# Performance work log

Hardware: AMD Instinct MI355X
Metric: run time of the kernel (lower is better)

Reference implementation:

```python
import math
import jax, jax.numpy as jnp
import numpy as np

NQ, NK = 16384, 4096
QDIM, KDIM, MID = 512, 256, 256


def setup_inputs() -> dict:
    key = jax.random.key(0)
    k1, k2, k3, k4, k5, k6, k7, k8 = jax.random.split(key, 8)
    return {
        "global_embeddings": jax.random.normal(k1, (NQ, QDIM), dtype=jnp.float32),
        "substruct_embeddings": jax.random.normal(k2, (NK, KDIM), dtype=jnp.float32),
        "substruct_weight": jax.random.uniform(k3, (NK,), dtype=jnp.float32),
        "mask": jax.random.randint(k4, (NQ, NK), 0, 2, dtype=jnp.int32),
        "Wq": jax.random.normal(k5, (MID, QDIM), dtype=jnp.float32) / math.sqrt(QDIM),
        "bq": jax.random.normal(k6, (MID,), dtype=jnp.float32) * 0.01,
        "Wk": jax.random.normal(k7, (MID, KDIM), dtype=jnp.float32) / math.sqrt(KDIM),
        "bk": jax.random.normal(k8, (MID,), dtype=jnp.float32) * 0.01,
    }


def reference(global_embeddings, substruct_embeddings, substruct_weight, mask, Wq, bq, Wk, bk):
    # Q/K projections (torch Linear: x @ W.T + b)
    Q = global_embeddings @ Wq.T + bq            # [NQ, MID]
    K = substruct_embeddings @ Wk.T + bk         # [NK, MID]
    scores = (Q @ K.T) / math.sqrt(MID)          # [NQ, NK]
    scores = jnp.where(mask == 0, -jnp.inf, scores)
    attn = jax.nn.softmax(scores, axis=-1)       # row-wise stable softmax
    # torch.diag(w) @ E  ==  elementwise row scaling
    V = substruct_weight[:, None] * substruct_embeddings  # [NK, KDIM]
    return attn @ V                              # [NQ, KDIM]
```

## Files before the change

kernel.cpp:

```cpp
#include <hip/hip_runtime.h>
#include <hip/hip_bf16.h>

typedef __bf16 bf16_t;
typedef bf16_t bf16x8 __attribute__((ext_vector_type(8)));
typedef float  f32x4  __attribute__((ext_vector_type(4)));
typedef unsigned long long u64;
typedef unsigned int u32;

#define MFMA16(A,B,C) __builtin_amdgcn_mfma_f32_16x16x32_bf16((A),(B),(C),0,0,0)


static __device__ __forceinline__ void gl_lds16(const bf16_t* g, void* l) {
    __builtin_amdgcn_global_load_lds(
        (const __attribute__((address_space(1))) u32*)(const void*)g,
        (__attribute__((address_space(3))) u32*)l, 16, 0, 0);
}

template<int KA, bool SWZ>
__global__ __launch_bounds__(256)
void proj_kernel(const float* __restrict__ A, const float* __restrict__ W,
                 const float* __restrict__ b, bf16_t* __restrict__ C,
                 float scale)
{
    __shared__ bf16_t Alds[64][40];
    __shared__ bf16_t Wlds[256][40];

    const int t  = threadIdx.x;
    const int w  = t >> 6, l = t & 63, lr = l & 15, lg = l >> 4;
    const int m0 = blockIdx.x * 64;

    f32x4 acc[16];
#pragma unroll
    for (int tt = 0; tt < 16; ++tt) acc[tt] = (f32x4){0.f, 0.f, 0.f, 0.f};

    const int ar  = t >> 2;
    const int ac8 = (t & 3) * 8;

    for (int kb = 0; kb < KA / 32; ++kb) {
        {
            const float* ap = A + (size_t)(m0 + ar) * KA + kb * 32 + ac8;
            float4 a0 = *(const float4*)ap;
            float4 a1 = *(const float4*)(ap + 4);
            bf16x8 av;
            av[0]=(bf16_t)a0.x; av[1]=(bf16_t)a0.y; av[2]=(bf16_t)a0.z; av[3]=(bf16_t)a0.w;
            av[4]=(bf16_t)a1.x; av[5]=(bf16_t)a1.y; av[6]=(bf16_t)a1.z; av[7]=(bf16_t)a1.w;
            *(bf16x8*)&Alds[ar][ac8] = av;
        }
#pragma unroll
        for (int c = 0; c < 4; ++c) {
            int e8 = c * 256 + t;
            int wr = e8 >> 2, wc8 = (e8 & 3) * 8;
            const float* wp = W + (size_t)wr * KA + kb * 32 + wc8;
            float4 w0 = *(const float4*)wp;
            float4 w1 = *(const float4*)(wp + 4);
            bf16x8 wv;
            wv[0]=(bf16_t)w0.x; wv[1]=(bf16_t)w0.y; wv[2]=(bf16_t)w0.z; wv[3]=(bf16_t)w0.w;
            wv[4]=(bf16_t)w1.x; wv[5]=(bf16_t)w1.y; wv[6]=(bf16_t)w1.z; wv[7]=(bf16_t)w1.w;
            *(bf16x8*)&Wlds[wr][wc8] = wv;
        }
        __syncthreads();

        bf16x8 af = *(bf16x8*)&Alds[w * 16 + lr][lg * 8];
#pragma unroll
        for (int tt = 0; tt < 16; ++tt) {
            bf16x8 bfrag = *(bf16x8*)&Wlds[tt * 16 + lr][lg * 8];
            acc[tt] = MFMA16(af, bfrag, acc[tt]);
        }
        __syncthreads();
    }

#pragma unroll
    for (int tt = 0; tt < 16; ++tt) {
        int col = tt * 16 + lr;
        float bias = b[col];
#pragma unroll
        for (int r = 0; r < 4; ++r) {
            int row = m0 + w * 16 + lg * 4 + r;
            int colS = col;
            if (SWZ) colS = (((col >> 3) ^ (row & 7)) << 3) | (col & 7);
            C[(size_t)row * 256 + colS] = (bf16_t)((acc[tt][r] + bias) * scale);
        }
    }
}

__global__ __launch_bounds__(256)
void buildvt_kernel(const float* __restrict__ S, const float* __restrict__ wgt,
                    bf16_t* __restrict__ VT)
{
    int i = blockIdx.x * 256 + threadIdx.x;
    int d = i >> 12, k = i & 4095;
    int kt = (k & ~63) | (((((k >> 3) & 7) ^ (d & 7)) << 3)) | (k & 7);
    VT[i] = (bf16_t)(wgt[kt] * S[(size_t)kt * 256 + d]);
}

template<bool SPLIT>
__global__ __launch_bounds__(512, 2)
void attn_kernel(const bf16_t* __restrict__ Qb, const bf16_t* __restrict__ Kb,
                 const bf16_t* __restrict__ VT, const int* __restrict__ mask,
                 float* __restrict__ out, float* __restrict__ pacc,
                 float* __restrict__ pm, float* __restrict__ pl)
{
    __shared__ __align__(16) char Kraw[2][32768];
    __shared__ __align__(16) char Vraw[2][32768];

    const int t  = threadIdx.x;
    const int w  = t >> 6, l = t & 63, lr = l & 15, lg = l >> 4;
    const int qw = blockIdx.x * 128 + w * 16;
    const int half = SPLIT ? (int)blockIdx.y : 0;
    const int NT   = SPLIT ? 32 : 64;
    const int kb0  = half * NT;

    bf16x8 qf[8];
    {
        const bf16_t* qrow = Qb + (size_t)(qw + lr) * 256;
#pragma unroll
        for (int kk = 0; kk < 8; ++kk)
            qf[kk] = *(const bf16x8*)(qrow + kk * 32 + lg * 8);
    }

    bf16x8 vone;
#pragma unroll
    for (int j = 0; j < 8; ++j) vone[j] = (bf16_t)1.0f;

    f32x4 acc[16];
#pragma unroll
    for (int dt = 0; dt < 16; ++dt) acc[dt] = (f32x4){0.f, 0.f, 0.f, 0.f};
    f32x4 lacc = (f32x4){0.f, 0.f, 0.f, 0.f};
    float mrow = -1e30f;
    bf16x8 pa[2];

    char* const K0 = &Kraw[0][0];
    char* const K1 = &Kraw[1][0];
    char* const V0 = &Vraw[0][0];
    char* const V1 = &Vraw[1][0];

    auto stageK = [&](int kb, char* kd) {
#pragma unroll
        for (int i = 0; i < 4; ++i) {
            int row = w * 8 + i * 2 + (l >> 5);
            gl_lds16(Kb + (size_t)(kb * 64 + row) * 256 + (l & 31) * 8,
                     kd + (w * 8 + i * 2) * 512);
        }
    };
    auto stageV = [&](int kb, char* vd) {
#pragma unroll
        for (int i = 0; i < 4; ++i) {
            int d = w * 32 + i * 8 + (l >> 3);
            gl_lds16(VT + (size_t)d * 4096 + kb * 64 + (l & 7) * 8,
                     vd + (w * 32 + i * 8) * 128);
        }
    };

    auto qk = [&](char* kcur, f32x4 (&s)[4]) {
#pragma unroll
        for (int tt = 0; tt < 4; ++tt) {
            f32x4 sv = (f32x4){0.f, 0.f, 0.f, 0.f};
#pragma unroll
            for (int kk = 0; kk < 8; ++kk) {
                bf16x8 kf = *(bf16x8*)(kcur + (((tt * 16 + lr) * 512)
                                | ((((kk * 4 + lg) ^ (lr & 7)) << 4))));
                sv = MFMA16(kf, qf[kk], sv);
            }
            s[tt] = sv;
        }
    };

    auto pv = [&](char* vcur) {
        lacc = MFMA16(pa[0], vone, lacc);
        lacc = MFMA16(pa[1], vone, lacc);
#pragma unroll
        for (int dt = 0; dt < 16; ++dt) {
            int vrow = dt * 16 + lr;
            bf16x8 v0 = *(bf16x8*)(vcur + ((vrow * 128)
                            | ((((0 * 4 + lg) ^ (lr & 7)) << 4))));
            bf16x8 v1 = *(bf16x8*)(vcur + ((vrow * 128)
                            | ((((1 * 4 + lg) ^ (lr & 7)) << 4))));
            acc[dt] = MFMA16(pa[0], v0, acc[dt]);
            acc[dt] = MFMA16(pa[1], v1, acc[dt]);
        }
    };

    auto softmax = [&](int4 (&mv)[4], f32x4 (&s)[4]) {
#pragma unroll
        for (int tt = 0; tt < 4; ++tt) {
            s[tt][0] = mv[tt].x ? s[tt][0] : -1e30f;
            s[tt][1] = mv[tt].y ? s[tt][1] : -1e30f;
            s[tt][2] = mv[tt].z ? s[tt][2] : -1e30f;
            s[tt][3] = mv[tt].w ? s[tt][3] : -1e30f;
        }
        float bm;
        {
            f32x4 m4 = s[0];
#pragma unroll
            for (int tt = 1; tt < 4; ++tt) {
                m4[0] = fmaxf(m4[0], s[tt][0]);
                m4[1] = fmaxf(m4[1], s[tt][1]);
                m4[2] = fmaxf(m4[2], s[tt][2]);
                m4[3] = fmaxf(m4[3], s[tt][3]);
            }
            bm = fmaxf(fmaxf(m4[0], m4[1]), fmaxf(m4[2], m4[3]));
            bm = fmaxf(bm, __shfl_xor(bm, 16));
            bm = fmaxf(bm, __shfl_xor(bm, 32));
        }
        bool need = bm > mrow + 8.f;
        if (__any(need)) {
            float mn = fmaxf(mrow, bm);
            float fr = __expf(mrow - mn);
            mrow = mn;
            float frC[4];
#pragma unroll
            for (int r = 0; r < 4; ++r) frC[r] = __shfl(fr, lg * 4 + r);
#pragma unroll
            for (int r = 0; r < 4; ++r) {
                lacc[r] *= frC[r];
#pragma unroll
                for (int dt = 0; dt < 16; ++dt) acc[dt][r] *= frC[r];
            }
        }
#pragma unroll
        for (int tt = 0; tt < 4; ++tt)
#pragma unroll
            for (int r = 0; r < 4; ++r)
                s[tt][r] = __expf(s[tt][r] - mrow);

#pragma unroll
        for (int g = 0; g < 2; ++g) {
            u32 x0, x1, y0, y1;
            asm("v_cvt_pk_bf16_f32 %0, %1, %2"
                : "=v"(x0) : "v"(s[2 * g][0]), "v"(s[2 * g][1]));
            asm("v_cvt_pk_bf16_f32 %0, %1, %2"
                : "=v"(x1) : "v"(s[2 * g][2]), "v"(s[2 * g][3]));
            asm("v_cvt_pk_bf16_f32 %0, %1, %2"
                : "=v"(y0) : "v"(s[2 * g + 1][0]), "v"(s[2 * g + 1][1]));
            asm("v_cvt_pk_bf16_f32 %0, %1, %2"
                : "=v"(y1) : "v"(s[2 * g + 1][2]), "v"(s[2 * g + 1][3]));
            asm volatile("v_permlane32_swap_b32 %0, %1" : "+v"(x0), "+v"(y0));
            asm volatile("v_permlane32_swap_b32 %0, %1" : "+v"(x1), "+v"(y1));
            u32 sx0 = (u32)__shfl_xor((int)x0, 16);
            u32 sx1 = (u32)__shfl_xor((int)x1, 16);
            u32 sy0 = (u32)__shfl_xor((int)y0, 16);
            u32 sy1 = (u32)__shfl_xor((int)y1, 16);
            bool evn = (lg & 1) == 0;
            union { u32 uw[4]; bf16x8 v; } pu;
            pu.uw[0] = evn ? x0  : sy0;
            pu.uw[1] = evn ? x1  : sy1;
            pu.uw[2] = evn ? sx0 : y0;
            pu.uw[3] = evn ? sx1 : y1;
            pa[g] = pu.v;
        }
    };

    stageK(kb0, K0);
    stageV(kb0, V0);
    __syncthreads();
    {
        int4 mv[4];
#pragma unroll
        for (int tt = 0; tt < 4; ++tt)
            mv[tt] = *(const int4*)(mask + (size_t)(qw + lr) * 4096
                                    + kb0 * 64 + tt * 16 + lg * 4);
        f32x4 s[4];
        qk(K0, s);
        softmax(mv, s);
    }
    stageK(kb0 + 1, K1);
    __syncthreads();

    for (int tb = 0; tb < NT - 1; ++tb) {
        char* kQ = (tb & 1) ? K0 : K1;
        char* vP = (tb & 1) ? V1 : V0;
        char* kS = (tb & 1) ? K1 : K0;
        char* vS = (tb & 1) ? V0 : V1;
        const int kb = kb0 + tb;

        int4 mv[4];
#pragma unroll
        for (int tt = 0; tt < 4; ++tt)
            mv[tt] = *(const int4*)(mask + (size_t)(qw + lr) * 4096
                                    + (kb + 1) * 64 + tt * 16 + lg * 4);

        if (tb + 2 < NT) stageK(kb + 2, kS);
        stageV(kb + 1, vS);

        __builtin_amdgcn_s_setprio(1);
        f32x4 s[4];
        qk(kQ, s);
        pv(vP);
        __builtin_amdgcn_s_setprio(0);

        softmax(mv, s);

        __syncthreads();
    }

    {
        char* vP = ((NT - 1) & 1) ? V1 : V0;
        pv(vP);
    }

    if (SPLIT) {
        float* pa_ = pacc + (size_t)half * 16384 * 256;
#pragma unroll
        for (int r = 0; r < 4; ++r) {
            int row = qw + lg * 4 + r;
#pragma unroll
            for (int dt = 0; dt < 16; ++dt)
                pa_[(size_t)row * 256 + dt * 16 + lr] = acc[dt][r];
            if (lr == 0) pl[half * 16384 + row] = lacc[r];
        }
        if (l < 16) pm[half * 16384 + qw + lr] = mrow;
    } else {
#pragma unroll
        for (int r = 0; r < 4; ++r) {
            float inv = 1.0f / lacc[r];
#pragma unroll
            for (int dt = 0; dt < 16; ++dt)
                out[(size_t)(qw + lg * 4 + r) * 256 + dt * 16 + lr]
                    = acc[dt][r] * inv;
        }
    }
}

__global__ __launch_bounds__(256)
void combine_kernel(const float* __restrict__ pacc, const float* __restrict__ pm,
                    const float* __restrict__ pl, float* __restrict__ out)
{
    int idx = blockIdx.x * 256 + threadIdx.x;
    int row = idx >> 6, c4 = (idx & 63) * 4;
    float m0 = pm[row], m1 = pm[16384 + row];
    float l0 = pl[row], l1 = pl[16384 + row];
    float m  = fmaxf(m0, m1);
    float a  = __expf(m0 - m), b = __expf(m1 - m);
    float inv = 1.0f / (l0 * a + l1 * b);
    float4 x0 = *(const float4*)(pacc + (size_t)row * 256 + c4);
    float4 x1 = *(const float4*)(pacc + (size_t)16384 * 256 + (size_t)row * 256 + c4);
    float4 o;
    o.x = (x0.x * a + x1.x * b) * inv;
    o.y = (x0.y * a + x1.y * b) * inv;
    o.z = (x0.z * a + x1.z * b) * inv;
    o.w = (x0.w * a + x1.w * b) * inv;
    *(float4*)(out + (size_t)row * 256 + c4) = o;
}

extern "C" void kernel_launch(void* const* d_in, const int* in_sizes, int n_in,
                              void* d_out, int out_size, void* d_ws, size_t ws_size,
                              hipStream_t stream)
{
    const float* gE   = (const float*)d_in[0];
    const float* sE   = (const float*)d_in[1];
    const float* wgt  = (const float*)d_in[2];
    const int*   mask = (const int*)  d_in[3];
    const float* Wq   = (const float*)d_in[4];
    const float* bq   = (const float*)d_in[5];
    const float* Wk   = (const float*)d_in[6];
    const float* bk   = (const float*)d_in[7];
    float* out = (float*)d_out;

    char* ws = (char*)d_ws;
    bf16_t* Qb = (bf16_t*)ws;
    bf16_t* Kb = (bf16_t*)(ws + 8388608);
    bf16_t* VT = (bf16_t*)(ws + 10485760);
    float*  pacc = (float*)(ws + 12582912);
    float*  pm   = (float*)(ws + 46137344);
    float*  pl   = (float*)(ws + 46268416);
    const size_t need_full = 46399488;
    const size_t need_min  = 12582912;

    if (ws_size < need_min) return;

    proj_kernel<512, false><<<dim3(256, 1), 256, 0, stream>>>(gE, Wq, bq, Qb, 0.0625f);
    proj_kernel<256, true ><<<dim3(64, 1), 256, 0, stream>>>(sE, Wk, bk, Kb, 1.0f);
    buildvt_kernel<<<4096, 256, 0, stream>>>(sE, wgt, VT);

    if (ws_size >= need_full) {
        attn_kernel<true><<<dim3(128, 2), 512, 0, stream>>>(
            Qb, Kb, VT, mask, out, pacc, pm, pl);
        combine_kernel<<<4096, 256, 0, stream>>>(pacc, pm, pl, out);
    } else {
        attn_kernel<false><<<dim3(128, 1), 512, 0, stream>>>(
            Qb, Kb, VT, mask, out, nullptr, nullptr, nullptr);
    }
}
```

Baseline: 187.7 us.

## Shrink attention tiles to 64 queries and 32 keys with pre-tiled V layout

```diff
diff --git a/kernel.cpp b/kernel.cpp
--- a/kernel.cpp
+++ b/kernel.cpp
@@ -85,29 +85,32 @@
 
 __global__ __launch_bounds__(256)
 void buildvt_kernel(const float* __restrict__ S, const float* __restrict__ wgt,
-                    bf16_t* __restrict__ VT)
+                    bf16_t* __restrict__ VTg)
 {
     int i = blockIdx.x * 256 + threadIdx.x;
-    int d = i >> 12, k = i & 4095;
-    int kt = (k & ~63) | (((((k >> 3) & 7) ^ (d & 7)) << 3)) | (k & 7);
-    VT[i] = (bf16_t)(wgt[kt] * S[(size_t)kt * 256 + d]);
+    int kb = i >> 13;
+    int c  = (i >> 11) & 3;
+    int d  = (i >> 3) & 255;
+    int j  = i & 7;
+    int k  = kb * 32 + c * 8 + j;
+    VTg[i] = (bf16_t)(wgt[k] * S[(size_t)k * 256 + d]);
 }
 
 template<bool SPLIT>
-__global__ __launch_bounds__(512, 2)
+__global__ __launch_bounds__(256, 2)
 void attn_kernel(const bf16_t* __restrict__ Qb, const bf16_t* __restrict__ Kb,
-                 const bf16_t* __restrict__ VT, const int* __restrict__ mask,
+                 const bf16_t* __restrict__ VTg, const int* __restrict__ mask,
                  float* __restrict__ out, float* __restrict__ pacc,
                  float* __restrict__ pm, float* __restrict__ pl)
 {
-    __shared__ __align__(16) char Kraw[2][32768];
-    __shared__ __align__(16) char Vraw[2][32768];
+    __shared__ __align__(16) char Kraw[2][16384];
+    __shared__ __align__(16) char Vraw[2][16384];
 
     const int t  = threadIdx.x;
     const int w  = t >> 6, l = t & 63, lr = l & 15, lg = l >> 4;
-    const int qw = blockIdx.x * 128 + w * 16;
+    const int qw = blockIdx.x * 64 + w * 16;
     const int half = SPLIT ? (int)blockIdx.y : 0;
-    const int NT   = SPLIT ? 32 : 64;
+    const int NT   = SPLIT ? 64 : 128;
     const int kb0  = half * NT;
 
     bf16x8 qf[8];
@@ -127,7 +130,7 @@
     for (int dt = 0; dt < 16; ++dt) acc[dt] = (f32x4){0.f, 0.f, 0.f, 0.f};
     f32x4 lacc = (f32x4){0.f, 0.f, 0.f, 0.f};
     float mrow = -1e30f;
-    bf16x8 pa[2];
+    bf16x8 pa;
 
     char* const K0 = &Kraw[0][0];
     char* const K1 = &Kraw[1][0];
@@ -138,22 +141,21 @@
 #pragma unroll
         for (int i = 0; i < 4; ++i) {
             int row = w * 8 + i * 2 + (l >> 5);
-            gl_lds16(Kb + (size_t)(kb * 64 + row) * 256 + (l & 31) * 8,
+            gl_lds16(Kb + (size_t)(kb * 32 + row) * 256 + (l & 31) * 8,
                      kd + (w * 8 + i * 2) * 512);
         }
     };
     auto stageV = [&](int kb, char* vd) {
 #pragma unroll
         for (int i = 0; i < 4; ++i) {
-            int d = w * 32 + i * 8 + (l >> 3);
-            gl_lds16(VT + (size_t)d * 4096 + kb * 64 + (l & 7) * 8,
-                     vd + (w * 32 + i * 8) * 128);
-        }
-    };
-
-    auto qk = [&](char* kcur, f32x4 (&s)[4]) {
-#pragma unroll
-        for (int tt = 0; tt < 4; ++tt) {
+            gl_lds16(VTg + (size_t)kb * 8192 + w * 2048 + i * 512 + l * 8,
+                     vd + w * 4096 + i * 1024);
+        }
+    };
+
+    auto qk = [&](char* kcur, f32x4 (&s)[2]) {
+#pragma unroll
+        for (int tt = 0; tt < 2; ++tt) {
             f32x4 sv = (f32x4){0.f, 0.f, 0.f, 0.f};
 #pragma unroll
             for (int kk = 0; kk < 8; ++kk) {
@@ -166,23 +168,17 @@
     };
 
     auto pv = [&](char* vcur) {
-        lacc = MFMA16(pa[0], vone, lacc);
-        lacc = MFMA16(pa[1], vone, lacc);
+        lacc = MFMA16(pa, vone, lacc);
 #pragma unroll
         for (int dt = 0; dt < 16; ++dt) {
-            int vrow = dt * 16 + lr;
-            bf16x8 v0 = *(bf16x8*)(vcur + ((vrow * 128)
-                            | ((((0 * 4 + lg) ^ (lr & 7)) << 4))));
-            bf16x8 v1 = *(bf16x8*)(vcur + ((vrow * 128)
-                            | ((((1 * 4 + lg) ^ (lr & 7)) << 4))));
-            acc[dt] = MFMA16(pa[0], v0, acc[dt]);
-            acc[dt] = MFMA16(pa[1], v1, acc[dt]);
-        }
-    };
-
-    auto softmax = [&](int4 (&mv)[4], f32x4 (&s)[4]) {
-#pragma unroll
-        for (int tt = 0; tt < 4; ++tt) {
+            bf16x8 vf = *(bf16x8*)(vcur + lg * 4096 + (dt * 16 + lr) * 16);
+            acc[dt] = MFMA16(pa, vf, acc[dt]);
+        }
+    };
+
+    auto softmax = [&](int4 (&mv)[2], f32x4 (&s)[2]) {
+#pragma unroll
+        for (int tt = 0; tt < 2; ++tt) {
             s[tt][0] = mv[tt].x ? s[tt][0] : -1e30f;
             s[tt][1] = mv[tt].y ? s[tt][1] : -1e30f;
             s[tt][2] = mv[tt].z ? s[tt][2] : -1e30f;
@@ -190,14 +186,11 @@
         }
         float bm;
         {
-            f32x4 m4 = s[0];
-#pragma unroll
-            for (int tt = 1; tt < 4; ++tt) {
-                m4[0] = fmaxf(m4[0], s[tt][0]);
-                m4[1] = fmaxf(m4[1], s[tt][1]);
-                m4[2] = fmaxf(m4[2], s[tt][2]);
-                m4[3] = fmaxf(m4[3], s[tt][3]);
-            }
+            f32x4 m4;
+            m4[0] = fmaxf(s[0][0], s[1][0]);
+            m4[1] = fmaxf(s[0][1], s[1][1]);
+            m4[2] = fmaxf(s[0][2], s[1][2]);
+            m4[3] = fmaxf(s[0][3], s[1][3]);
             bm = fmaxf(fmaxf(m4[0], m4[1]), fmaxf(m4[2], m4[3]));
             bm = fmaxf(bm, __shfl_xor(bm, 16));
             bm = fmaxf(bm, __shfl_xor(bm, 32));
@@ -218,22 +211,21 @@
             }
         }
 #pragma unroll
-        for (int tt = 0; tt < 4; ++tt)
+        for (int tt = 0; tt < 2; ++tt)
 #pragma unroll
             for (int r = 0; r < 4; ++r)
                 s[tt][r] = __expf(s[tt][r] - mrow);
 
-#pragma unroll
-        for (int g = 0; g < 2; ++g) {
+        {
             u32 x0, x1, y0, y1;
             asm("v_cvt_pk_bf16_f32 %0, %1, %2"
-                : "=v"(x0) : "v"(s[2 * g][0]), "v"(s[2 * g][1]));
+                : "=v"(x0) : "v"(s[0][0]), "v"(s[0][1]));
             asm("v_cvt_pk_bf16_f32 %0, %1, %2"
-                : "=v"(x1) : "v"(s[2 * g][2]), "v"(s[2 * g][3]));
+                : "=v"(x1) : "v"(s[0][2]), "v"(s[0][3]));
             asm("v_cvt_pk_bf16_f32 %0, %1, %2"
-                : "=v"(y0) : "v"(s[2 * g + 1][0]), "v"(s[2 * g + 1][1]));
+                : "=v"(y0) : "v"(s[1][0]), "v"(s[1][1]));
             asm("v_cvt_pk_bf16_f32 %0, %1, %2"
-                : "=v"(y1) : "v"(s[2 * g + 1][2]), "v"(s[2 * g + 1][3]));
+                : "=v"(y1) : "v"(s[1][2]), "v"(s[1][3]));
             asm volatile("v_permlane32_swap_b32 %0, %1" : "+v"(x0), "+v"(y0));
             asm volatile("v_permlane32_swap_b32 %0, %1" : "+v"(x1), "+v"(y1));
             u32 sx0 = (u32)__shfl_xor((int)x0, 16);
@@ -246,20 +238,20 @@
             pu.uw[1] = evn ? x1  : sy1;
             pu.uw[2] = evn ? sx0 : y0;
             pu.uw[3] = evn ? sx1 : y1;
-            pa[g] = pu.v;
-        }
-    };
-
+            pa = pu.v;
+        }
+    };
+
+    stageV(kb0, V0);
     stageK(kb0, K0);
-    stageV(kb0, V0);
     __syncthreads();
     {
-        int4 mv[4];
-#pragma unroll
-        for (int tt = 0; tt < 4; ++tt)
+        int4 mv[2];
+#pragma unroll
+        for (int tt = 0; tt < 2; ++tt)
             mv[tt] = *(const int4*)(mask + (size_t)(qw + lr) * 4096
-                                    + kb0 * 64 + tt * 16 + lg * 4);
-        f32x4 s[4];
+                                    + kb0 * 32 + tt * 16 + lg * 4);
+        f32x4 s[2];
         qk(K0, s);
         softmax(mv, s);
     }
@@ -273,17 +265,17 @@
         char* vS = (tb & 1) ? V0 : V1;
         const int kb = kb0 + tb;
 
-        int4 mv[4];
-#pragma unroll
-        for (int tt = 0; tt < 4; ++tt)
+        int4 mv[2];
+#pragma unroll
+        for (int tt = 0; tt < 2; ++tt)
             mv[tt] = *(const int4*)(mask + (size_t)(qw + lr) * 4096
-                                    + (kb + 1) * 64 + tt * 16 + lg * 4);
-
+                                    + (kb + 1) * 32 + tt * 16 + lg * 4);
+
+        stageV(kb + 1, vS);
         if (tb + 2 < NT) stageK(kb + 2, kS);
-        stageV(kb + 1, vS);
 
         __builtin_amdgcn_s_setprio(1);
-        f32x4 s[4];
+        f32x4 s[2];
         qk(kQ, s);
         pv(vP);
         __builtin_amdgcn_s_setprio(0);
@@ -373,11 +365,11 @@
     buildvt_kernel<<<4096, 256, 0, stream>>>(sE, wgt, VT);
 
     if (ws_size >= need_full) {
-        attn_kernel<true><<<dim3(128, 2), 512, 0, stream>>>(
+        attn_kernel<true><<<dim3(256, 2), 256, 0, stream>>>(
             Qb, Kb, VT, mask, out, pacc, pm, pl);
         combine_kernel<<<4096, 256, 0, stream>>>(pacc, pm, pl, out);
     } else {
-        attn_kernel<false><<<dim3(128, 1), 512, 0, stream>>>(
+        attn_kernel<false><<<dim3(256, 1), 256, 0, stream>>>(
             Qb, Kb, VT, mask, out, nullptr, nullptr, nullptr);
     }
 }
```

After: 178.7 us. -4.8%, faster.
